# Optimization experiments

Measured on AMD Instinct MI355X. Metric: run time of the kernel, lower is better.

The kernel has to match this reference:

```python
import jax, jax.numpy as jnp
import numpy as np

NUM_HEADS = 16
HEAD_DIM = 64
DIM = NUM_HEADS * HEAD_DIM
ROPE_BASE = 10000.0
EPS = 1e-6


def rotate_half(x):
    # pairs (x0,x1) -> (-x1, x0), interleaved on last dim
    x_even = x[..., ::2]
    x_odd = x[..., 1::2]
    return jnp.stack((-x_odd, x_even), axis=-1).reshape(x.shape)


def apply_rope(q, k, positions, base=ROPE_BASE):
    d = q.shape[-1]
    inv_freq = 1.0 / (base ** (jnp.arange(0, d, 2, dtype=jnp.float32) / d))
    angles = positions.astype(jnp.float32)[..., None] * inv_freq  # [B, L, d/2]
    cos = jnp.repeat(jnp.cos(angles), 2, axis=-1).astype(q.dtype)[:, None, :, :]  # [B,1,L,d]
    sin = jnp.repeat(jnp.sin(angles), 2, axis=-1).astype(q.dtype)[:, None, :, :]
    return q * cos + rotate_half(q) * sin, k * cos + rotate_half(k) * sin


def per_head_layernorm(x, weight):
    # x: [B, H, L, d]; weight: [H, d]; bias is zeros (qkv_bias=False)
    mu = jnp.mean(x, axis=-1, keepdims=True)
    var = jnp.mean(jnp.square(x - mu), axis=-1, keepdims=True)
    xn = (x - mu) * jax.lax.rsqrt(var + EPS)
    return xn * weight[None, :, None, :]


def setup_inputs() -> dict:
    key = jax.random.key(0)
    k1, k2, k3, k4, k5 = jax.random.split(key, 5)
    B, L = 2, 2048
    x = jax.random.normal(k1, (B, L, DIM), dtype=jnp.float32)
    mask = jnp.ones((B, L, L), dtype=bool)
    positions = jnp.broadcast_to(jnp.arange(L, dtype=jnp.int64 if jax.config.jax_enable_x64 else jnp.int32), (B, L))
    s = 1.0 / np.sqrt(DIM)
    W_qkv = jax.random.normal(k2, (DIM, 3 * DIM), dtype=jnp.float32) * s
    W_out = jax.random.normal(k3, (DIM, DIM), dtype=jnp.float32) * s
    qn_w = jnp.ones((NUM_HEADS, HEAD_DIM), dtype=jnp.float32)
    kn_w = jnp.ones((NUM_HEADS, HEAD_DIM), dtype=jnp.float32)
    return {"x": x, "mask": mask, "positions": positions,
            "W_qkv": W_qkv, "W_out": W_out, "qn_w": qn_w, "kn_w": kn_w}


def reference(x, mask, positions, W_qkv, W_out, qn_w, kn_w):
    B, L, D = x.shape
    scale = HEAD_DIM ** -0.5
    qkv = x @ W_qkv  # [B, L, 3D]
    qkv = qkv.reshape(B, L, 3, NUM_HEADS, HEAD_DIM)
    qkv = jnp.transpose(qkv, (2, 0, 3, 1, 4))  # [3, B, H, L, d]
    q, k, v = qkv[0], qkv[1], qkv[2]
    q = per_head_layernorm(q, qn_w)
    k = per_head_layernorm(k, kn_w)
    q, k = apply_rope(q, k, positions)
    attn = jnp.einsum('bhqd,bhkd->bhqk', q, k) * scale  # [B, H, L, L]
    attn = jnp.where(mask[:, None, :, :], attn, -jnp.inf)
    attn = jax.nn.softmax(attn, axis=-1)
    out = jnp.einsum('bhqk,bhkd->bhqd', attn, v)  # [B, H, L, d]
    out = jnp.transpose(out, (0, 2, 1, 3)).reshape(B, L, D)
    return out @ W_out
```

## Files before the change

### kernel.cpp

```cpp
#include <hip/hip_runtime.h>


typedef __bf16 bf16x8 __attribute__((ext_vector_type(8)));
typedef __bf16 bf16x2 __attribute__((ext_vector_type(2)));
typedef float f32x4 __attribute__((ext_vector_type(4)));

#define QSCALE 0.1803368802f

__device__ __forceinline__ float bf2f(unsigned short u) {
  unsigned int v = ((unsigned int)u) << 16;
  float f;
  __builtin_memcpy(&f, &v, 4);
  return f;
}
__device__ __forceinline__ unsigned short f2bf(float f) {
  unsigned int v;
  __builtin_memcpy(&v, &f, 4);
  v += 0x7fffu + ((v >> 16) & 1u);
  return (unsigned short)(v >> 16);
}
__device__ __forceinline__ unsigned short f2bf_hw(float f) {
  __bf16 h = (__bf16)f;
  unsigned short u;
  __builtin_memcpy(&u, &h, 2);
  return u;
}
__device__ __forceinline__ unsigned int pack2(float a, float b) {
  bf16x2 t;
  t[0] = (__bf16)a;
  t[1] = (__bf16)b;
  unsigned int u;
  __builtin_memcpy(&u, &t, 4);
  return u;
}
__device__ __forceinline__ void gl_lds16(const unsigned short* g, unsigned short* l) {
  __builtin_amdgcn_global_load_lds(
      (const __attribute__((address_space(1))) unsigned int*)g,
      (__attribute__((address_space(3))) unsigned int*)l, 16, 0, 0);
}

__global__ __launch_bounds__(256) void prep(
    const float* __restrict__ x, const float* __restrict__ W_qkv,
    const float* __restrict__ W_out, const int* __restrict__ positions,
    unsigned short* __restrict__ xb,
    unsigned short* __restrict__ Wt_qkv, unsigned short* __restrict__ Wt_out,
    float2* __restrict__ lut) {
  __shared__ float tile[64][65];
  const int bid = blockIdx.x, t = threadIdx.x;
  if (bid < 4096) {
    int i = (bid * 256 + t) * 4;
    float4 v = *reinterpret_cast<const float4*>(x + i);
    ushort4 o;
    o.x = f2bf(v.x); o.y = f2bf(v.y); o.z = f2bf(v.z); o.w = f2bf(v.w);
    *reinterpret_cast<ushort4*>(xb + i) = o;
    return;
  }
  if (bid >= 5120) {
    int idx = (bid - 5120) * 256 + t;
    int m = idx >> 5, p = idx & 31;
    float pos = (float)positions[m];
    float invf = __builtin_amdgcn_exp2f(-(float)(2 * p) * (13.2877124f / 64.0f));
    float rev = pos * invf * 0.15915494f;
    rev -= floorf(rev);
    lut[idx] = make_float2(__builtin_amdgcn_cosf(rev), __builtin_amdgcn_sinf(rev));
    return;
  }
  const float* W; unsigned short* Wt; int Nd, bn, bk;
  if (bid < 4864) {
    int id = bid - 4096; W = W_qkv; Wt = Wt_qkv; Nd = 3072; bn = id % 48; bk = id / 48;
  } else {
    int id = bid - 4864; W = W_out; Wt = Wt_out; Nd = 1024; bn = id % 16; bk = id / 16;
  }
  const int Kd = 1024;
#pragma unroll
  for (int i = 0; i < 16; i++) {
    int idx = i * 256 + t;
    int k = idx >> 6, n = idx & 63;
    tile[k][n] = W[(size_t)(bk * 64 + k) * Nd + bn * 64 + n];
  }
  __syncthreads();
#pragma unroll
  for (int i = 0; i < 16; i++) {
    int idx = i * 256 + t;
    int n = idx >> 6, k = idx & 63;
    Wt[(size_t)(bn * 64 + n) * Kd + bk * 64 + k] = f2bf(tile[k][n]);
  }
}

__global__ __launch_bounds__(256) void gemm_qkv(
    const unsigned short* __restrict__ A,
    const unsigned short* __restrict__ Bt,
    const float* __restrict__ qn_w, const float* __restrict__ kn_w,
    const float2* __restrict__ lut,
    unsigned short* __restrict__ Qr,
    unsigned short* __restrict__ Kr,
    unsigned short* __restrict__ Vt, int K) {
  __shared__ __align__(16) unsigned short As[2][128 * 32];
  __shared__ __align__(16) unsigned short Bs[2][128 * 32];
  const int tid = threadIdx.x;
  const int lane = tid & 63, wid = tid >> 6;
  const int quad = lane >> 4, l16 = lane & 15;
  const int wr = wid >> 1, wc = wid & 1;
  const int bn = blockIdx.x, bm = blockIdx.y;
  const unsigned short* Ab = A + (size_t)bm * 128 * K;
  const unsigned short* Bb = Bt + (size_t)bn * 128 * K;

  f32x4 acc[4][4] = {};

  const int c0 = tid, c1 = tid + 256;
  const int ar0 = c0 >> 2, ag0 = ((c0 & 3) ^ ((ar0 >> 1) & 3)) * 8;
  const int ar1 = c1 >> 2, ag1 = ((c1 & 3) ^ ((ar1 >> 1) & 3)) * 8;

  gl_lds16(Ab + (size_t)ar0 * K + ag0, &As[0][c0 * 8]);
  gl_lds16(Ab + (size_t)ar1 * K + ag1, &As[0][c1 * 8]);
  gl_lds16(Bb + (size_t)ar0 * K + ag0, &Bs[0][c0 * 8]);
  gl_lds16(Bb + (size_t)ar1 * K + ag1, &Bs[0][c1 * 8]);

  const int iters = K >> 5;
  for (int it = 0; it < iters; it++) {
    const int cur = it & 1;
    __builtin_amdgcn_s_barrier();
    if (it + 1 < iters) {
      const int k0 = (it + 1) << 5, nb = cur ^ 1;
      gl_lds16(Ab + (size_t)ar0 * K + k0 + ag0, &As[nb][c0 * 8]);
      gl_lds16(Ab + (size_t)ar1 * K + k0 + ag1, &As[nb][c1 * 8]);
      gl_lds16(Bb + (size_t)ar0 * K + k0 + ag0, &Bs[nb][c0 * 8]);
      gl_lds16(Bb + (size_t)ar1 * K + k0 + ag1, &Bs[nb][c1 * 8]);
      __builtin_amdgcn_sched_barrier(0);
      asm volatile("s_waitcnt vmcnt(4)" ::: "memory");
    } else {
      __builtin_amdgcn_sched_barrier(0);
      asm volatile("s_waitcnt vmcnt(0)" ::: "memory");
    }
    __builtin_amdgcn_sched_barrier(0);
    const unsigned short* Ac = As[cur];
    const unsigned short* Bc = Bs[cur];
    bf16x8 af[4], bfr[4];
#pragma unroll
    for (int i = 0; i < 4; i++) {
      int m = wr * 64 + i * 16 + l16;
      af[i] = *reinterpret_cast<const bf16x8*>(&Ac[m * 32 + ((quad ^ ((m >> 1) & 3)) * 8)]);
    }
#pragma unroll
    for (int j = 0; j < 4; j++) {
      int n = wc * 64 + j * 16 + l16;
      bfr[j] = *reinterpret_cast<const bf16x8*>(&Bc[n * 32 + ((quad ^ ((n >> 1) & 3)) * 8)]);
    }
#pragma unroll
    for (int i = 0; i < 4; i++)
#pragma unroll
      for (int j = 0; j < 4; j++)
        acc[i][j] = __builtin_amdgcn_mfma_f32_16x16x32_bf16(af[i], bfr[j], acc[i][j], 0, 0, 0);
  }

  const int sec = bn >> 3;
  const int h = (bn & 7) * 2 + wc;
  const int b = bm >> 4;
  if (sec < 2) {
    const float* gw = sec ? kn_w : qn_w;
    unsigned short* dst = sec ? Kr : Qr;
    const float oscale = sec ? 1.0f : QSCALE;
    float w4[4];
#pragma unroll
    for (int j = 0; j < 4; j++) w4[j] = gw[h * 64 + j * 16 + l16];
#pragma unroll
    for (int i = 0; i < 4; i++)
#pragma unroll
      for (int r = 0; r < 4; r++) {
        int m = bm * 128 + wr * 64 + i * 16 + quad * 4 + r;
        int l = m & 2047;
        const float2* lrow = lut + m * 32;
        float2 cs4[4];
#pragma unroll
        for (int j = 0; j < 4; j++) cs4[j] = lrow[j * 8 + (l16 >> 1)];
        float sum = acc[i][0][r] + acc[i][1][r] + acc[i][2][r] + acc[i][3][r];
        float sq = acc[i][0][r] * acc[i][0][r] + acc[i][1][r] * acc[i][1][r] +
                   acc[i][2][r] * acc[i][2][r] + acc[i][3][r] * acc[i][3][r];
#pragma unroll
        for (int off = 1; off < 16; off <<= 1) {
          sum += __shfl_xor(sum, off);
          sq += __shfl_xor(sq, off);
        }
        float mu = sum * (1.0f / 64.0f);
        float var = sq * (1.0f / 64.0f) - mu * mu;
        float rs = rsqrtf(fmaxf(var, 0.0f) + 1e-6f);
#pragma unroll
        for (int j = 0; j < 4; j++) {
          float y = (acc[i][j][r] - mu) * rs * w4[j];
          float p = __shfl_xor(y, 1);
          float o = (l16 & 1) ? (y * cs4[j].x + p * cs4[j].y)
                              : (y * cs4[j].x - p * cs4[j].y);
          dst[((size_t)(b * 16 + h) * 2048 + l) * 64 + j * 16 + l16] = f2bf(o * oscale);
        }
      }
  } else {
#pragma unroll
    for (int i = 0; i < 4; i++) {
      int lp = (bm * 128 + wr * 64 + (i >> 1) * 32 + quad * 8 + (i & 1) * 4) & 2047;
#pragma unroll
      for (int j = 0; j < 4; j++) {
        int d = j * 16 + l16;
        uint2 v;
        v.x = pack2(acc[i][j][0], acc[i][j][1]);
        v.y = pack2(acc[i][j][2], acc[i][j][3]);
        *reinterpret_cast<uint2*>(&Vt[((size_t)(b * 16 + h) * 64 + d) * 2048 + lp]) = v;
      }
    }
  }
}

__global__ __launch_bounds__(512, 4) void attn_kernel(
    const unsigned short* __restrict__ Q,
    const unsigned short* __restrict__ K,
    const unsigned short* __restrict__ Vt,
    unsigned short* __restrict__ O) {
  __shared__ __align__(16) unsigned short Ks[2][2][64 * 64];
  __shared__ __align__(16) unsigned short Vs[2][2][64 * 64];

  int bid = blockIdx.x;
  int id = (bid & 7) * 64 + (bid >> 3);
  const int qt = id & 15; id >>= 4;
  const int h = id & 15;  const int b = id >> 4;
  const int tid = threadIdx.x;
  const int lane = tid & 63, wid = tid >> 6;
  const int half = wid >> 2, wg = wid & 3;
  const int quad = lane >> 4, l16 = lane & 15;

  const unsigned short* Qb = Q + (size_t)(b * 16 + h) * 2048 * 64;
  const unsigned short* Kb = K + (size_t)(b * 16 + h) * 2048 * 64;
  const unsigned short* Vb = Vt + (size_t)(b * 16 + h) * 64 * 2048;

  const int qbase = qt * 128 + wg * 32;
  bf16x8 qf[2][2];
#pragma unroll
  for (int g = 0; g < 2; g++)
#pragma unroll
    for (int d = 0; d < 2; d++)
      qf[g][d] = *reinterpret_cast<const bf16x8*>(
          &Qb[(size_t)(qbase + g * 16 + l16) * 64 + d * 32 + quad * 8]);

  bf16x8 ones8;
#pragma unroll
  for (int i = 0; i < 8; i++) ones8[i] = (__bf16)1.0f;

  f32x4 o[2][4] = {};
  f32x4 lacc[2] = {};

  const int ltid = tid & 255;
  const int c0 = ltid, c1 = ltid + 256;
  const int r0 = c0 >> 3, g0 = ((c0 & 7) ^ (r0 & 7)) * 8;
  const int r1 = c1 >> 3, g1 = ((c1 & 7) ^ (r1 & 7)) * 8;
  const int kb0 = half * 1024;

  gl_lds16(&Kb[(size_t)(kb0 + r0) * 64 + g0], &Ks[half][0][c0 * 8]);
  gl_lds16(&Kb[(size_t)(kb0 + r1) * 64 + g1], &Ks[half][0][c1 * 8]);
  gl_lds16(&Vb[(size_t)r0 * 2048 + kb0 + g0], &Vs[half][0][c0 * 8]);
  gl_lds16(&Vb[(size_t)r1 * 2048 + kb0 + g1], &Vs[half][0][c1 * 8]);

  for (int kt = 0; kt < 16; kt++) {
    const int cur = kt & 1;
    __builtin_amdgcn_s_barrier();
    if (kt + 1 < 16) {
      const int ko = kb0 + (kt + 1) * 64, nb = cur ^ 1;
      gl_lds16(&Kb[(size_t)(ko + r0) * 64 + g0], &Ks[half][nb][c0 * 8]);
      gl_lds16(&Kb[(size_t)(ko + r1) * 64 + g1], &Ks[half][nb][c1 * 8]);
      gl_lds16(&Vb[(size_t)r0 * 2048 + ko + g0], &Vs[half][nb][c0 * 8]);
      gl_lds16(&Vb[(size_t)r1 * 2048 + ko + g1], &Vs[half][nb][c1 * 8]);
      __builtin_amdgcn_sched_barrier(0);
      asm volatile("s_waitcnt vmcnt(4)" ::: "memory");
    } else {
      __builtin_amdgcn_sched_barrier(0);
      asm volatile("s_waitcnt vmcnt(0)" ::: "memory");
    }
    __builtin_amdgcn_sched_barrier(0);
    const unsigned short* Kc = Ks[half][cur];
    const unsigned short* Vc = Vs[half][cur];

    bf16x8 kf[4][2];
#pragma unroll
    for (int kg = 0; kg < 4; kg++)
#pragma unroll
      for (int d = 0; d < 2; d++) {
        int row = kg * 16 + l16;
        kf[kg][d] = *reinterpret_cast<const bf16x8*>(
            &Kc[row * 64 + (((d * 4 + quad) ^ (row & 7)) * 8)]);
      }
    bf16x8 vf[4][2];
#pragma unroll
    for (int i = 0; i < 4; i++)
#pragma unroll
      for (int c = 0; c < 2; c++) {
        int row = i * 16 + l16;
        vf[i][c] = *reinterpret_cast<const bf16x8*>(
            &Vc[row * 64 + (((c * 4 + quad) ^ (row & 7)) * 8)]);
      }

#pragma unroll
    for (int g = 0; g < 2; g++) {
      f32x4 s4[4] = {};
#pragma unroll
      for (int kg = 0; kg < 4; kg++) {
        s4[kg] = __builtin_amdgcn_mfma_f32_16x16x32_bf16(kf[kg][0], qf[g][0], s4[kg], 0, 0, 0);
        s4[kg] = __builtin_amdgcn_mfma_f32_16x16x32_bf16(kf[kg][1], qf[g][1], s4[kg], 0, 0, 0);
      }
      float pv[4][4];
#pragma unroll
      for (int kg = 0; kg < 4; kg++)
#pragma unroll
        for (int r = 0; r < 4; r++)
          pv[kg][r] = __builtin_amdgcn_exp2f(s4[kg][r]);
#pragma unroll
      for (int c = 0; c < 2; c++) {
        union { unsigned int u[4]; bf16x8 v; } pa;
        pa.u[0] = pack2(pv[c * 2][0], pv[c * 2][1]);
        pa.u[1] = pack2(pv[c * 2][2], pv[c * 2][3]);
        pa.u[2] = pack2(pv[c * 2 + 1][0], pv[c * 2 + 1][1]);
        pa.u[3] = pack2(pv[c * 2 + 1][2], pv[c * 2 + 1][3]);
        lacc[g] = __builtin_amdgcn_mfma_f32_16x16x32_bf16(pa.v, ones8, lacc[g], 0, 0, 0);
#pragma unroll
        for (int i = 0; i < 4; i++)
          o[g][i] = __builtin_amdgcn_mfma_f32_16x16x32_bf16(pa.v, vf[i][c], o[g][i], 0, 0, 0);
      }
    }
  }

  __syncthreads();
  float* Om = (float*)&Ks[0][0][0];
  float* Lm = (float*)&Vs[0][0][0];
  if (half == 0) {
#pragma unroll
    for (int g = 0; g < 2; g++) {
#pragma unroll
      for (int i = 0; i < 4; i++)
#pragma unroll
        for (int r = 0; r < 4; r++)
          Om[(wg * 32 + g * 16 + quad * 4 + r) * 64 + i * 16 + l16] = o[g][i][r];
      if (l16 == 0) {
#pragma unroll
        for (int r = 0; r < 4; r++)
          Lm[wg * 32 + g * 16 + quad * 4 + r] = lacc[g][r];
      }
    }
  }
  __syncthreads();
  if (half == 1) {
#pragma unroll
    for (int g = 0; g < 2; g++) {
#pragma unroll
      for (int r = 0; r < 4; r++) {
        float lt = lacc[g][r] + Lm[wg * 32 + g * 16 + quad * 4 + r];
        float inv = 1.0f / lt;
        int q = qbase + g * 16 + quad * 4 + r;
#pragma unroll
        for (int i = 0; i < 4; i++) {
          float sum = o[g][i][r] + Om[(wg * 32 + g * 16 + quad * 4 + r) * 64 + i * 16 + l16];
          O[((size_t)(b * 2048 + q)) * 1024 + h * 64 + i * 16 + l16] = f2bf_hw(sum * inv);
        }
      }
    }
  }
}

__global__ __launch_bounds__(256) void gemm_out(
    const unsigned short* __restrict__ A,
    const unsigned short* __restrict__ Bt,
    float* __restrict__ C, int M, int N, int K) {
  __shared__ __align__(16) unsigned short As[2][128 * 32];
  __shared__ __align__(16) unsigned short Bs[2][64 * 32];
  const int tid = threadIdx.x;
  const int lane = tid & 63, wid = tid >> 6;
  const int quad = lane >> 4, l16 = lane & 15;
  const int bn = blockIdx.x, bm = blockIdx.y;
  const unsigned short* Ab = A + (size_t)bm * 128 * K;
  const unsigned short* Bb = Bt + (size_t)bn * 64 * K;

  f32x4 acc[2][4] = {};

  const int c0 = tid, c1 = tid + 256;
  const int ar0 = c0 >> 2, ag0 = ((c0 & 3) ^ ((ar0 >> 1) & 3)) * 8;
  const int ar1 = c1 >> 2, ag1 = ((c1 & 3) ^ ((ar1 >> 1) & 3)) * 8;
  const int br = tid >> 2, bg = ((tid & 3) ^ ((br >> 1) & 3)) * 8;

  gl_lds16(Ab + (size_t)ar0 * K + ag0, &As[0][c0 * 8]);
  gl_lds16(Ab + (size_t)ar1 * K + ag1, &As[0][c1 * 8]);
  gl_lds16(Bb + (size_t)br * K + bg, &Bs[0][tid * 8]);

  const int iters = K >> 5;
  for (int it = 0; it < iters; it++) {
    const int cur = it & 1;
    __builtin_amdgcn_s_barrier();
    if (it + 1 < iters) {
      const int k0 = (it + 1) << 5, nb = cur ^ 1;
      gl_lds16(Ab + (size_t)ar0 * K + k0 + ag0, &As[nb][c0 * 8]);
      gl_lds16(Ab + (size_t)ar1 * K + k0 + ag1, &As[nb][c1 * 8]);
      gl_lds16(Bb + (size_t)br * K + k0 + bg, &Bs[nb][tid * 8]);
      __builtin_amdgcn_sched_barrier(0);
      asm volatile("s_waitcnt vmcnt(3)" ::: "memory");
    } else {
      __builtin_amdgcn_sched_barrier(0);
      asm volatile("s_waitcnt vmcnt(0)" ::: "memory");
    }
    __builtin_amdgcn_sched_barrier(0);
    const unsigned short* Ac = As[cur];
    const unsigned short* Bc = Bs[cur];
    bf16x8 af[2], bfr[4];
#pragma unroll
    for (int i = 0; i < 2; i++) {
      int m = wid * 32 + i * 16 + l16;
      af[i] = *reinterpret_cast<const bf16x8*>(&Ac[m * 32 + ((quad ^ ((m >> 1) & 3)) * 8)]);
    }
#pragma unroll
    for (int j = 0; j < 4; j++) {
      int n = j * 16 + l16;
      bfr[j] = *reinterpret_cast<const bf16x8*>(&Bc[n * 32 + ((quad ^ ((n >> 1) & 3)) * 8)]);
    }
#pragma unroll
    for (int i = 0; i < 2; i++)
#pragma unroll
      for (int j = 0; j < 4; j++)
        acc[i][j] = __builtin_amdgcn_mfma_f32_16x16x32_bf16(af[i], bfr[j], acc[i][j], 0, 0, 0);
  }
#pragma unroll
  for (int i = 0; i < 2; i++)
#pragma unroll
    for (int j = 0; j < 4; j++)
#pragma unroll
      for (int r = 0; r < 4; r++) {
        int m = bm * 128 + wid * 32 + i * 16 + quad * 4 + r;
        int n = bn * 64 + j * 16 + l16;
        C[(size_t)m * N + n] = acc[i][j][r];
      }
}

extern "C" void kernel_launch(void* const* d_in, const int* in_sizes, int n_in,
                              void* d_out, int out_size, void* d_ws, size_t ws_size,
                              hipStream_t stream) {
  (void)in_sizes; (void)n_in; (void)out_size; (void)ws_size;
  const float* x     = (const float*)d_in[0];
  const int*   pos   = (const int*)d_in[2];
  const float* W_qkv = (const float*)d_in[3];
  const float* W_out = (const float*)d_in[4];
  const float* qn_w  = (const float*)d_in[5];
  const float* kn_w  = (const float*)d_in[6];
  float*       out   = (float*)d_out;

  char* ws = (char*)d_ws;
  unsigned short* xb     = (unsigned short*)(ws);
  unsigned short* Qr     = (unsigned short*)(ws + 8388608);
  unsigned short* Kr     = (unsigned short*)(ws + 16777216);
  unsigned short* Vt     = (unsigned short*)(ws + 25165824);
  unsigned short* Wt_qkv = (unsigned short*)(ws + 33554432);
  unsigned short* Wt_out = (unsigned short*)(ws + 39845888);
  float2*         lut    = (float2*)(ws + 41943040);
  unsigned short* attn_o = xb;

  prep<<<5632, 256, 0, stream>>>(x, W_qkv, W_out, pos, xb, Wt_qkv, Wt_out, lut);
  gemm_qkv<<<dim3(24, 32), 256, 0, stream>>>(xb, Wt_qkv, qn_w, kn_w, lut, Qr, Kr, Vt, 1024);
  attn_kernel<<<512, 512, 0, stream>>>(Qr, Kr, Vt, attn_o);
  gemm_out<<<dim3(16, 32), 256, 0, stream>>>(attn_o, Wt_out, out, 4096, 1024, 1024);
}
```

Before: 207.9 us.

## Triple-buffer GEMM LDS pipelines and interleave attention MFMA groups with raised priority

Both GEMM kernels move from double to triple LDS buffering, prefetching two k-tiles ahead with adjusted vmcnt waits to hide more global-load latency. The attention inner loop is restructured to compute both query groups' QK^T together, load K fragments inline and V fragments on demand, and raise wave priority with s_setprio around the MFMA section. The extra LDS per block may reduce occupancy, and the rescheduled attention loop changes register pressure.

Result: faster. 200.0 us (-3.8%).

```diff
diff --git a/kernel.cpp b/kernel.cpp
--- a/kernel.cpp
+++ b/kernel.cpp
@@ -95,8 +95,8 @@
     unsigned short* __restrict__ Qr,
     unsigned short* __restrict__ Kr,
     unsigned short* __restrict__ Vt, int K) {
-  __shared__ __align__(16) unsigned short As[2][128 * 32];
-  __shared__ __align__(16) unsigned short Bs[2][128 * 32];
+  __shared__ __align__(16) unsigned short As[3][128 * 32];
+  __shared__ __align__(16) unsigned short Bs[3][128 * 32];
   const int tid = threadIdx.x;
   const int lane = tid & 63, wid = tid >> 6;
   const int quad = lane >> 4, l16 = lane & 15;
@@ -115,17 +115,24 @@
   gl_lds16(Ab + (size_t)ar1 * K + ag1, &As[0][c1 * 8]);
   gl_lds16(Bb + (size_t)ar0 * K + ag0, &Bs[0][c0 * 8]);
   gl_lds16(Bb + (size_t)ar1 * K + ag1, &Bs[0][c1 * 8]);
+  gl_lds16(Ab + (size_t)ar0 * K + 32 + ag0, &As[1][c0 * 8]);
+  gl_lds16(Ab + (size_t)ar1 * K + 32 + ag1, &As[1][c1 * 8]);
+  gl_lds16(Bb + (size_t)ar0 * K + 32 + ag0, &Bs[1][c0 * 8]);
+  gl_lds16(Bb + (size_t)ar1 * K + 32 + ag1, &Bs[1][c1 * 8]);
 
   const int iters = K >> 5;
+  int cur = 0, nxt = 2;
   for (int it = 0; it < iters; it++) {
-    const int cur = it & 1;
     __builtin_amdgcn_s_barrier();
-    if (it + 1 < iters) {
-      const int k0 = (it + 1) << 5, nb = cur ^ 1;
-      gl_lds16(Ab + (size_t)ar0 * K + k0 + ag0, &As[nb][c0 * 8]);
-      gl_lds16(Ab + (size_t)ar1 * K + k0 + ag1, &As[nb][c1 * 8]);
-      gl_lds16(Bb + (size_t)ar0 * K + k0 + ag0, &Bs[nb][c0 * 8]);
-      gl_lds16(Bb + (size_t)ar1 * K + k0 + ag1, &Bs[nb][c1 * 8]);
+    if (it + 2 < iters) {
+      const int k0 = (it + 2) << 5;
+      gl_lds16(Ab + (size_t)ar0 * K + k0 + ag0, &As[nxt][c0 * 8]);
+      gl_lds16(Ab + (size_t)ar1 * K + k0 + ag1, &As[nxt][c1 * 8]);
+      gl_lds16(Bb + (size_t)ar0 * K + k0 + ag0, &Bs[nxt][c0 * 8]);
+      gl_lds16(Bb + (size_t)ar1 * K + k0 + ag1, &Bs[nxt][c1 * 8]);
+      __builtin_amdgcn_sched_barrier(0);
+      asm volatile("s_waitcnt vmcnt(8)" ::: "memory");
+    } else if (it + 1 < iters) {
       __builtin_amdgcn_sched_barrier(0);
       asm volatile("s_waitcnt vmcnt(4)" ::: "memory");
     } else {
@@ -151,6 +158,8 @@
 #pragma unroll
       for (int j = 0; j < 4; j++)
         acc[i][j] = __builtin_amdgcn_mfma_f32_16x16x32_bf16(af[i], bfr[j], acc[i][j], 0, 0, 0);
+    cur = (cur == 2) ? 0 : cur + 1;
+    nxt = (nxt == 2) ? 0 : nxt + 1;
   }
 
   const int sec = bn >> 3;
@@ -276,52 +285,55 @@
     const unsigned short* Kc = Ks[half][cur];
     const unsigned short* Vc = Vs[half][cur];
 
-    bf16x8 kf[4][2];
+    __builtin_amdgcn_s_setprio(1);
+    f32x4 s4a[4] = {}, s4b[4] = {};
+#pragma unroll
+    for (int kg = 0; kg < 4; kg++) {
+      int row = kg * 16 + l16;
+      bf16x8 kf0 = *reinterpret_cast<const bf16x8*>(
+          &Kc[row * 64 + ((quad ^ (row & 7)) * 8)]);
+      bf16x8 kf1 = *reinterpret_cast<const bf16x8*>(
+          &Kc[row * 64 + (((4 + quad) ^ (row & 7)) * 8)]);
+      s4a[kg] = __builtin_amdgcn_mfma_f32_16x16x32_bf16(kf0, qf[0][0], s4a[kg], 0, 0, 0);
+      s4a[kg] = __builtin_amdgcn_mfma_f32_16x16x32_bf16(kf1, qf[0][1], s4a[kg], 0, 0, 0);
+      s4b[kg] = __builtin_amdgcn_mfma_f32_16x16x32_bf16(kf0, qf[1][0], s4b[kg], 0, 0, 0);
+      s4b[kg] = __builtin_amdgcn_mfma_f32_16x16x32_bf16(kf1, qf[1][1], s4b[kg], 0, 0, 0);
+    }
+    float pva[4][4], pvb[4][4];
 #pragma unroll
     for (int kg = 0; kg < 4; kg++)
 #pragma unroll
-      for (int d = 0; d < 2; d++) {
-        int row = kg * 16 + l16;
-        kf[kg][d] = *reinterpret_cast<const bf16x8*>(
-            &Kc[row * 64 + (((d * 4 + quad) ^ (row & 7)) * 8)]);
-      }
-    bf16x8 vf[4][2];
-#pragma unroll
-    for (int i = 0; i < 4; i++)
-#pragma unroll
-      for (int c = 0; c < 2; c++) {
+      for (int r = 0; r < 4; r++) {
+        pva[kg][r] = __builtin_amdgcn_exp2f(s4a[kg][r]);
+        pvb[kg][r] = __builtin_amdgcn_exp2f(s4b[kg][r]);
+      }
+    union u32x4v { unsigned int u[4]; bf16x8 v; };
+    u32x4v paa[2], pab[2];
+#pragma unroll
+    for (int c = 0; c < 2; c++) {
+      paa[c].u[0] = pack2(pva[c * 2][0], pva[c * 2][1]);
+      paa[c].u[1] = pack2(pva[c * 2][2], pva[c * 2][3]);
+      paa[c].u[2] = pack2(pva[c * 2 + 1][0], pva[c * 2 + 1][1]);
+      paa[c].u[3] = pack2(pva[c * 2 + 1][2], pva[c * 2 + 1][3]);
+      pab[c].u[0] = pack2(pvb[c * 2][0], pvb[c * 2][1]);
+      pab[c].u[1] = pack2(pvb[c * 2][2], pvb[c * 2][3]);
+      pab[c].u[2] = pack2(pvb[c * 2 + 1][0], pvb[c * 2 + 1][1]);
+      pab[c].u[3] = pack2(pvb[c * 2 + 1][2], pvb[c * 2 + 1][3]);
+    }
+#pragma unroll
+    for (int c = 0; c < 2; c++) {
+      lacc[0] = __builtin_amdgcn_mfma_f32_16x16x32_bf16(paa[c].v, ones8, lacc[0], 0, 0, 0);
+      lacc[1] = __builtin_amdgcn_mfma_f32_16x16x32_bf16(pab[c].v, ones8, lacc[1], 0, 0, 0);
+#pragma unroll
+      for (int i = 0; i < 4; i++) {
         int row = i * 16 + l16;
-        vf[i][c] = *reinterpret_cast<const bf16x8*>(
+        bf16x8 vfr = *reinterpret_cast<const bf16x8*>(
             &Vc[row * 64 + (((c * 4 + quad) ^ (row & 7)) * 8)]);
-      }
-
-#pragma unroll
-    for (int g = 0; g < 2; g++) {
-      f32x4 s4[4] = {};
-#pragma unroll
-      for (int kg = 0; kg < 4; kg++) {
-        s4[kg] = __builtin_amdgcn_mfma_f32_16x16x32_bf16(kf[kg][0], qf[g][0], s4[kg], 0, 0, 0);
-        s4[kg] = __builtin_amdgcn_mfma_f32_16x16x32_bf16(kf[kg][1], qf[g][1], s4[kg], 0, 0, 0);
-      }
-      float pv[4][4];
-#pragma unroll
-      for (int kg = 0; kg < 4; kg++)
-#pragma unroll
-        for (int r = 0; r < 4; r++)
-          pv[kg][r] = __builtin_amdgcn_exp2f(s4[kg][r]);
-#pragma unroll
-      for (int c = 0; c < 2; c++) {
-        union { unsigned int u[4]; bf16x8 v; } pa;
-        pa.u[0] = pack2(pv[c * 2][0], pv[c * 2][1]);
-        pa.u[1] = pack2(pv[c * 2][2], pv[c * 2][3]);
-        pa.u[2] = pack2(pv[c * 2 + 1][0], pv[c * 2 + 1][1]);
-        pa.u[3] = pack2(pv[c * 2 + 1][2], pv[c * 2 + 1][3]);
-        lacc[g] = __builtin_amdgcn_mfma_f32_16x16x32_bf16(pa.v, ones8, lacc[g], 0, 0, 0);
-#pragma unroll
-        for (int i = 0; i < 4; i++)
-          o[g][i] = __builtin_amdgcn_mfma_f32_16x16x32_bf16(pa.v, vf[i][c], o[g][i], 0, 0, 0);
-      }
-    }
+        o[0][i] = __builtin_amdgcn_mfma_f32_16x16x32_bf16(paa[c].v, vfr, o[0][i], 0, 0, 0);
+        o[1][i] = __builtin_amdgcn_mfma_f32_16x16x32_bf16(pab[c].v, vfr, o[1][i], 0, 0, 0);
+      }
+    }
+    __builtin_amdgcn_s_setprio(0);
   }
 
   __syncthreads();
@@ -365,8 +377,8 @@
     const unsigned short* __restrict__ A,
     const unsigned short* __restrict__ Bt,
     float* __restrict__ C, int M, int N, int K) {
-  __shared__ __align__(16) unsigned short As[2][128 * 32];
-  __shared__ __align__(16) unsigned short Bs[2][64 * 32];
+  __shared__ __align__(16) unsigned short As[3][128 * 32];
+  __shared__ __align__(16) unsigned short Bs[3][64 * 32];
   const int tid = threadIdx.x;
   const int lane = tid & 63, wid = tid >> 6;
   const int quad = lane >> 4, l16 = lane & 15;
@@ -384,16 +396,22 @@
   gl_lds16(Ab + (size_t)ar0 * K + ag0, &As[0][c0 * 8]);
   gl_lds16(Ab + (size_t)ar1 * K + ag1, &As[0][c1 * 8]);
   gl_lds16(Bb + (size_t)br * K + bg, &Bs[0][tid * 8]);
+  gl_lds16(Ab + (size_t)ar0 * K + 32 + ag0, &As[1][c0 * 8]);
+  gl_lds16(Ab + (size_t)ar1 * K + 32 + ag1, &As[1][c1 * 8]);
+  gl_lds16(Bb + (size_t)br * K + 32 + bg, &Bs[1][tid * 8]);
 
   const int iters = K >> 5;
+  int cur = 0, nxt = 2;
   for (int it = 0; it < iters; it++) {
-    const int cur = it & 1;
     __builtin_amdgcn_s_barrier();
-    if (it + 1 < iters) {
-      const int k0 = (it + 1) << 5, nb = cur ^ 1;
-      gl_lds16(Ab + (size_t)ar0 * K + k0 + ag0, &As[nb][c0 * 8]);
-      gl_lds16(Ab + (size_t)ar1 * K + k0 + ag1, &As[nb][c1 * 8]);
-      gl_lds16(Bb + (size_t)br * K + k0 + bg, &Bs[nb][tid * 8]);
+    if (it + 2 < iters) {
+      const int k0 = (it + 2) << 5;
+      gl_lds16(Ab + (size_t)ar0 * K + k0 + ag0, &As[nxt][c0 * 8]);
+      gl_lds16(Ab + (size_t)ar1 * K + k0 + ag1, &As[nxt][c1 * 8]);
+      gl_lds16(Bb + (size_t)br * K + k0 + bg, &Bs[nxt][tid * 8]);
+      __builtin_amdgcn_sched_barrier(0);
+      asm volatile("s_waitcnt vmcnt(6)" ::: "memory");
+    } else if (it + 1 < iters) {
       __builtin_amdgcn_sched_barrier(0);
       asm volatile("s_waitcnt vmcnt(3)" ::: "memory");
     } else {
@@ -419,6 +437,8 @@
 #pragma unroll
       for (int j = 0; j < 4; j++)
         acc[i][j] = __builtin_amdgcn_mfma_f32_16x16x32_bf16(af[i], bfr[j], acc[i][j], 0, 0, 0);
+    cur = (cur == 2) ? 0 : cur + 1;
+    nxt = (nxt == 2) ? 0 : nxt + 1;
   }
 #pragma unroll
   for (int i = 0; i < 2; i++)
```
